# Kernel tuning notes

Measured on AMD Instinct MI355X. Metric: run time of the kernel, lower is better.

## Reference

```python
import jax, jax.numpy as jnp
import numpy as np

EMBED_DIM = 1024
NUM_HEADS = 16
LB_HEADS = 8
LA_HEADS = 8
HEAD_DIM = EMBED_DIM // NUM_HEADS


def setup_inputs() -> dict:
    key = jax.random.key(0)
    ks = jax.random.split(key, 8)
    B, T, F, D = 2, 16, 128, EMBED_DIM
    def xavier(k, shape):
        fan_out, fan_in = shape[-2], shape[-1]
        lim = float(np.sqrt(6.0 / (fan_in + fan_out)))
        return jax.random.uniform(k, shape, jnp.float32, -lim, lim)
    return {
        "x": jax.random.normal(ks[0], (B, T, F, D), jnp.float32),
        # stacked per-head Linear weights, torch layout (out=head_dim, in=D)
        "Wq_lb": xavier(ks[1], (LB_HEADS, HEAD_DIM, D)),
        "Wk_lb": xavier(ks[2], (LB_HEADS, HEAD_DIM, D)),
        "Wv_lb": xavier(ks[3], (LB_HEADS, HEAD_DIM, D)),
        "Wq_la": xavier(ks[4], (LA_HEADS, HEAD_DIM, D)),
        "Wk_la": xavier(ks[5], (LA_HEADS, HEAD_DIM, D)),
        "Wv_la": xavier(ks[6], (LA_HEADS, HEAD_DIM, D)),
        "Wo": xavier(ks[7], (D, D)),
    }


def _masked_attention(xf, Wq, Wk, Wv, lookahead):
    # xf: (B, N, D); W*: (H, E, D). Equivalent to per-head Linear then stack.
    q = jnp.einsum('bnd,hed->bhne', xf, Wq)
    k = jnp.einsum('bnd,hed->bhne', xf, Wk)
    v = jnp.einsum('bnd,hed->bhne', xf, Wv)
    scale = 1.0 / jnp.sqrt(jnp.asarray(q.shape[-1], q.dtype))
    s = jnp.einsum('bhqe,bhke->bhqk', q, k) * scale
    n = s.shape[-1]
    i = jnp.arange(n)
    # frame/patch divmod mask reduces to token-level (anti-)causal
    mask = (i[:, None] <= i[None, :]) if lookahead else (i[:, None] >= i[None, :])
    s = jnp.where(mask, s, jnp.finfo(s.dtype).min)
    p = jax.nn.softmax(s, axis=-1)
    return jnp.einsum('bhqk,bhke->bhqe', p, v)  # (B, H, N, E)


def reference(x, Wq_lb, Wk_lb, Wv_lb, Wq_la, Wk_la, Wv_la, Wo):
    B, T, F, D = x.shape
    xf = x.reshape(B, T * F, D)
    o_lb = _masked_attention(xf, Wq_lb, Wk_lb, Wv_lb, lookahead=False)
    o_la = _masked_attention(xf, Wq_la, Wk_la, Wv_la, lookahead=True)
    o = jnp.concatenate([o_lb, o_la], axis=1)          # (B, H, N, E)
    o = o.reshape(B, T * F, D)                          # NOTE: raw reshape, no head transpose (matches torch source)
    out = jnp.einsum('bnd,od->bno', o, Wo)
    return out.reshape(B, T, F, D)
```

## Files before the change

### kernel.cpp

```cpp
#include <hip/hip_runtime.h>
#include <hip/hip_bf16.h>

constexpr int B_    = 2;
constexpr int NTOK  = 2048;
constexpr int D_    = 1024;
constexpr int H_    = 16;
constexpr int E_    = 64;

using bf16_t = __bf16;
using bf16x8 = __attribute__((ext_vector_type(8))) __bf16;
using f32x4  = __attribute__((ext_vector_type(4))) float;

#define NEG_BIG  (-30000.0f)
#define QSCALE   (0.125f * 1.44269504088896f)

__device__ __forceinline__ void load16_to_lds(const void* g, void* l) {
  __builtin_amdgcn_global_load_lds((const __attribute__((address_space(1))) void*)g,
                                   (__attribute__((address_space(3))) void*)l, 16, 0, 0);
}

__device__ __forceinline__ void stage64_async(const bf16_t* __restrict__ g, int gs,
                                              bf16_t* l, int tid) {
#pragma unroll
  for (int j = 0; j < 2; ++j) {
    int chunk = j * 256 + tid;
    int row = chunk >> 3, cc = chunk & 7;
    int gcc = cc ^ (row & 7);
    load16_to_lds(g + (long)row * gs + gcc * 8, l + chunk * 8);
  }
}

__device__ __forceinline__ void stage128x64_async(const bf16_t* __restrict__ g, int gs,
                                                  bf16_t* l, int tid) {
#pragma unroll
  for (int j = 0; j < 4; ++j) {
    int chunk = j * 256 + tid;
    int row = chunk >> 3, cc = chunk & 7;
    int gcc = cc ^ (row & 7);
    load16_to_lds(g + (long)row * gs + gcc * 8, l + chunk * 8);
  }
}

__device__ __forceinline__ bf16x8 frag_ld(const bf16_t* l, int row, int ks, int half) {
  int cc = (ks * 4 + half) ^ (row & 7);
  return *(const bf16x8*)&l[row * 64 + cc * 8];
}

__device__ __forceinline__ bf16x8 cvt8(f32x4 f0, f32x4 f1) {
  bf16x8 v;
  v[0] = (bf16_t)f0[0]; v[1] = (bf16_t)f0[1]; v[2] = (bf16_t)f0[2]; v[3] = (bf16_t)f0[3];
  v[4] = (bf16_t)f1[0]; v[5] = (bf16_t)f1[1]; v[6] = (bf16_t)f1[2]; v[7] = (bf16_t)f1[3];
  return v;
}

__global__ __launch_bounds__(256) void prep_kernel(
    const float* __restrict__ x,
    const float* __restrict__ q0, const float* __restrict__ q1,
    const float* __restrict__ k0, const float* __restrict__ k1,
    const float* __restrict__ v0, const float* __restrict__ v1,
    const float* __restrict__ wo,
    bf16_t* __restrict__ xb, bf16_t* __restrict__ Wb, bf16_t* __restrict__ Wob)
{
  const int bid = blockIdx.x;
  if (bid < 2048) {
    long i = ((long)bid * 256 + threadIdx.x) * 8;
    *(bf16x8*)&xb[i] = cvt8(*(const f32x4*)&x[i], *(const f32x4*)&x[i + 4]);
  } else if (bid < 3584) {
    int rb = bid - 2048;
    int sec = rb >> 5;
    int qkv = sec >> 4, hh = sec & 15;
    const float* s = (qkv == 0) ? (hh < 8 ? q0 : q1)
                   : (qkv == 1) ? (hh < 8 ? k0 : k1)
                                : (hh < 8 ? v0 : v1);
    s += (long)(hh & 7) * (E_ * D_);
    long off = ((long)(rb & 31) * 256 + threadIdx.x) * 8;
    *(bf16x8*)&Wb[(long)sec * (E_ * D_) + off] =
        cvt8(*(const f32x4*)&s[off], *(const f32x4*)&s[off + 4]);
  } else {
    long i = ((long)(bid - 3584) * 256 + threadIdx.x) * 8;
    *(bf16x8*)&Wob[i] = cvt8(*(const f32x4*)&wo[i], *(const f32x4*)&wo[i + 4]);
  }
}

__global__ __launch_bounds__(256) void qkv128_kernel(
    const bf16_t* __restrict__ xb, const bf16_t* __restrict__ Wb,
    bf16_t* __restrict__ Qb, bf16_t* __restrict__ Kb, bf16_t* __restrict__ Vt)
{
  __shared__ __align__(16) bf16_t smem[2 * 128 * 64];
  bf16_t* As = smem;
  bf16_t* Bs = smem + 128 * 64;

  const int tid = threadIdx.x;
  const int wv = tid >> 6, lane = tid & 63, lane16 = lane & 15, half = lane >> 4;
  const int wm = wv >> 1, wn = wv & 1;
  const int mt = blockIdx.x, nt = blockIdx.y;

  const bf16_t* Ag = xb + (long)mt * 128 * D_;
  const bf16_t* Bg = Wb + (long)nt * 128 * D_;

  f32x4 acc[4][4] = {};

  for (int k0 = 0; k0 < D_; k0 += 64) {
    __syncthreads();
    stage128x64_async(Ag + k0, D_, As, tid);
    stage128x64_async(Bg + k0, D_, Bs, tid);
    __syncthreads();
#pragma unroll
    for (int ks = 0; ks < 2; ++ks) {
      bf16x8 a[4], b[4];
#pragma unroll
      for (int i = 0; i < 4; ++i) a[i] = frag_ld(As, wm * 64 + i * 16 + lane16, ks, half);
#pragma unroll
      for (int i = 0; i < 4; ++i) b[i] = frag_ld(Bs, wn * 64 + i * 16 + lane16, ks, half);
#pragma unroll
      for (int mi = 0; mi < 4; ++mi)
#pragma unroll
        for (int ni = 0; ni < 4; ++ni)
          acc[mi][ni] = __builtin_amdgcn_mfma_f32_16x16x32_bf16(a[mi], b[ni], acc[mi][ni], 0, 0, 0);
    }
  }

  const int sec = nt >> 3;
  const int tok0 = mt * 128;
  const int b  = tok0 >> 11;
  const int n0 = tok0 & 2047;

  if (sec < 2) {
    const float qs = (sec == 0) ? QSCALE : 1.0f;
    bf16_t* dst = (sec == 0) ? Qb : Kb;
#pragma unroll
    for (int mi = 0; mi < 4; ++mi)
#pragma unroll
      for (int ni = 0; ni < 4; ++ni)
#pragma unroll
        for (int r = 0; r < 4; ++r) {
          int row  = wm * 64 + mi * 16 + half * 4 + r;
          int colg = nt * 128 + wn * 64 + ni * 16 + lane16;
          int cs = colg & 1023, h = cs >> 6, e = cs & 63;
          dst[((long)(b * H_ + h) * NTOK + n0 + row) * E_ + e] = (bf16_t)(acc[mi][ni][r] * qs);
        }
  } else {
#pragma unroll
    for (int c = 0; c < 2; ++c) {
      __syncthreads();
      if (wn == c) {
#pragma unroll
        for (int mi = 0; mi < 4; ++mi)
#pragma unroll
          for (int ni = 0; ni < 4; ++ni)
#pragma unroll
            for (int r = 0; r < 4; ++r) {
              int tok = wm * 64 + mi * 16 + half * 4 + r;
              int e   = ni * 16 + lane16;
              smem[e * 136 + tok] = (bf16_t)acc[mi][ni][r];
            }
      }
      __syncthreads();
      int hh = (nt & 7) * 2 + c;
      bf16_t* vdst = Vt + ((long)(b * H_ + hh) * E_) * NTOK;
#pragma unroll
      for (int q = 0; q < 4; ++q) {
        int chunk = q * 256 + tid;
        int e = chunk >> 4, toff = (chunk & 15) * 8;
        *(bf16x8*)&vdst[(long)e * NTOK + n0 + toff] = *(const bf16x8*)&smem[e * 136 + toff];
      }
    }
  }
}

__global__ __launch_bounds__(256) void attn_kernel(
    const bf16_t* __restrict__ Qb, const bf16_t* __restrict__ Kb,
    const bf16_t* __restrict__ Vt, bf16_t* __restrict__ Ob)
{
  __shared__ __align__(16) bf16_t Kl[2][64 * 64];
  __shared__ __align__(16) bf16_t Vl[2][64 * 64];
  __shared__ __align__(16) bf16_t Pl[2][64 * 72];

  const int tid = threadIdx.x;
  const int wv = tid >> 6, lane = tid & 63, lane16 = lane & 15, half = lane >> 4;
  const int qp = blockIdx.x, h = blockIdx.y, b = blockIdx.z;
  const bool causal = (h < 8);
  const int qb[2] = { qp, 31 - qp };
  const long bh = (long)(b * H_ + h);

  bf16x8 qf[2][2];
#pragma unroll
  for (int t = 0; t < 2; ++t) {
    const bf16_t* qg = Qb + (bh * NTOK + (long)qb[t] * 64 + 16 * wv + lane16) * E_;
    qf[t][0] = *(const bf16x8*)(qg + half * 8);
    qf[t][1] = *(const bf16x8*)(qg + 32 + half * 8);
  }

  f32x4 oacc[2][4] = {};
  float l_acc[2][4] = {};

  const int lo = causal ? 0 : qp;
  const int hi = causal ? 31 - qp : 31;

  stage64_async(Kb + (bh * NTOK + (long)lo * 64) * E_, E_, Kl[0], tid);
  stage64_async(Vt + bh * E_ * NTOK + (long)lo * 64, NTOK, Vl[0], tid);

  for (int kb = lo; kb <= hi; ++kb) {
    const int cur = (kb - lo) & 1;
    __syncthreads();
    if (kb < hi) {
      stage64_async(Kb + (bh * NTOK + (long)(kb + 1) * 64) * E_, E_, Kl[cur ^ 1], tid);
      stage64_async(Vt + bh * E_ * NTOK + (long)(kb + 1) * 64, NTOK, Vl[cur ^ 1], tid);
    }

#pragma unroll
    for (int t = 0; t < 2; ++t) {
      const bool act = causal ? (kb <= qb[t]) : (kb >= qb[t]);
      if (!act) continue;

      f32x4 s[4] = {};
#pragma unroll
      for (int ks = 0; ks < 2; ++ks)
#pragma unroll
        for (int n = 0; n < 4; ++n) {
          bf16x8 bk = frag_ld(Kl[cur], 16 * n + lane16, ks, half);
          s[n] = __builtin_amdgcn_mfma_f32_16x16x32_bf16(qf[t][ks], bk, s[n], 0, 0, 0);
        }

      if (kb == qb[t]) {
#pragma unroll
        for (int n = 0; n < 4; ++n) {
          int key = 16 * n + lane16;
#pragma unroll
          for (int r = 0; r < 4; ++r) {
            int q = 16 * wv + half * 4 + r;
            bool ok = causal ? (q >= key) : (q <= key);
            s[n][r] = ok ? s[n][r] : NEG_BIG;
          }
        }
      }

#pragma unroll
      for (int n = 0; n < 4; ++n)
#pragma unroll
        for (int r = 0; r < 4; ++r) {
          float p = exp2f(s[n][r]);
          s[n][r] = p;
          l_acc[t][r] += p;
        }

#pragma unroll
      for (int n = 0; n < 4; ++n)
#pragma unroll
        for (int r = 0; r < 4; ++r)
          Pl[t][(16 * wv + half * 4 + r) * 72 + 16 * n + lane16] = (bf16_t)s[n][r];
      asm volatile("" ::: "memory");

#pragma unroll
      for (int ks = 0; ks < 2; ++ks) {
        bf16x8 ap = *(const bf16x8*)&Pl[t][(16 * wv + lane16) * 72 + ks * 32 + half * 8];
#pragma unroll
        for (int n = 0; n < 4; ++n) {
          bf16x8 bv = frag_ld(Vl[cur], 16 * n + lane16, ks, half);
          oacc[t][n] = __builtin_amdgcn_mfma_f32_16x16x32_bf16(ap, bv, oacc[t][n], 0, 0, 0);
        }
      }
    }
  }

#pragma unroll
  for (int d = 1; d < 16; d <<= 1)
#pragma unroll
    for (int t = 0; t < 2; ++t)
#pragma unroll
      for (int r = 0; r < 4; ++r) l_acc[t][r] += __shfl_xor(l_acc[t][r], d, 64);

#pragma unroll
  for (int t = 0; t < 2; ++t) {
    bf16_t* og = Ob + (bh * NTOK + (long)qb[t] * 64) * E_;
#pragma unroll
    for (int r = 0; r < 4; ++r) {
      float rcp = 1.0f / l_acc[t][r];
      int row = 16 * wv + half * 4 + r;
#pragma unroll
      for (int n = 0; n < 4; ++n)
        og[(long)row * E_ + 16 * n + lane16] = (bf16_t)(oacc[t][n][r] * rcp);
    }
  }
}

__global__ __launch_bounds__(256) void oproj128_kernel(
    const bf16_t* __restrict__ Ob, const bf16_t* __restrict__ Wob,
    float* __restrict__ res)
{
  __shared__ __align__(16) bf16_t smem[2 * 128 * 64];
  bf16_t* As = smem;
  bf16_t* Bs = smem + 128 * 64;

  const int tid = threadIdx.x;
  const int wv = tid >> 6, lane = tid & 63, lane16 = lane & 15, half = lane >> 4;
  const int wm = wv >> 1, wn = wv & 1;
  const int mt = blockIdx.x, nt = blockIdx.y;

  const bf16_t* Ag = Ob  + (long)mt * 128 * D_;
  const bf16_t* Bg = Wob + (long)nt * 128 * D_;

  f32x4 acc[4][4] = {};

  for (int k0 = 0; k0 < D_; k0 += 64) {
    __syncthreads();
    stage128x64_async(Ag + k0, D_, As, tid);
    stage128x64_async(Bg + k0, D_, Bs, tid);
    __syncthreads();
#pragma unroll
    for (int ks = 0; ks < 2; ++ks) {
      bf16x8 a[4], b[4];
#pragma unroll
      for (int i = 0; i < 4; ++i) a[i] = frag_ld(As, wm * 64 + i * 16 + lane16, ks, half);
#pragma unroll
      for (int i = 0; i < 4; ++i) b[i] = frag_ld(Bs, wn * 64 + i * 16 + lane16, ks, half);
#pragma unroll
      for (int mi = 0; mi < 4; ++mi)
#pragma unroll
        for (int ni = 0; ni < 4; ++ni)
          acc[mi][ni] = __builtin_amdgcn_mfma_f32_16x16x32_bf16(a[mi], b[ni], acc[mi][ni], 0, 0, 0);
    }
  }

#pragma unroll
  for (int mi = 0; mi < 4; ++mi)
#pragma unroll
    for (int ni = 0; ni < 4; ++ni)
#pragma unroll
      for (int r = 0; r < 4; ++r) {
        int row = mt * 128 + wm * 64 + mi * 16 + half * 4 + r;
        int col = nt * 128 + wn * 64 + ni * 16 + lane16;
        res[(long)row * D_ + col] = acc[mi][ni][r];
      }
}

__global__ __launch_bounds__(256) void copy_kernel(const float* __restrict__ src,
                                                   float* __restrict__ dst) {
  long i = ((long)blockIdx.x * 256 + threadIdx.x) * 8;
  *(f32x4*)&dst[i]     = *(const f32x4*)&src[i];
  *(f32x4*)&dst[i + 4] = *(const f32x4*)&src[i + 4];
}

extern "C" void kernel_launch(void* const* d_in, const int* in_sizes, int n_in,
                              void* d_out, int out_size, void* d_ws, size_t ws_size,
                              hipStream_t stream) {
  const float* x     = (const float*)d_in[0];
  const float* wq_lb = (const float*)d_in[1];
  const float* wk_lb = (const float*)d_in[2];
  const float* wv_lb = (const float*)d_in[3];
  const float* wq_la = (const float*)d_in[4];
  const float* wk_la = (const float*)d_in[5];
  const float* wv_la = (const float*)d_in[6];
  const float* wo    = (const float*)d_in[7];
  float* out = (float*)d_out;

  const size_t per_buf = (size_t)B_ * H_ * NTOK * E_;

  bf16_t* Qb = (bf16_t*)d_ws;
  bf16_t* Kb = Qb + per_buf;
  bf16_t* Vt = Kb + per_buf;
  float*  res = (float*)d_ws;

  bf16_t* xb  = (bf16_t*)d_out;
  bf16_t* Wb  = xb + per_buf;
  bf16_t* Wob = Wb + (size_t)3 * 1024 * 1024;
  bf16_t* Ob  = (bf16_t*)d_out;

  prep_kernel<<<4096, 256, 0, stream>>>(x, wq_lb, wq_la, wk_lb, wk_la,
                                        wv_lb, wv_la, wo, xb, Wb, Wob);
  qkv128_kernel<<<dim3(32, 24), 256, 0, stream>>>(xb, Wb, Qb, Kb, Vt);
  attn_kernel<<<dim3(16, 16, 2), 256, 0, stream>>>(Qb, Kb, Vt, Ob);
  oproj128_kernel<<<dim3(32, 8), 256, 0, stream>>>(Ob, Wob, res);
  copy_kernel<<<2048, 256, 0, stream>>>(res, out);
}
```

Before: 212.8 us.

## Swap MFMA operands to get transposed accumulators and vectorize epilogue stores

Swaps the A/B operands of the MFMA calls in the Q/K projection, attention and output projection, so each lane's four accumulator values lie along the contiguous feature dimension. Stores then become 4-wide vector writes (bf16x4 or f32x4) instead of scalar scattered writes. In attention, the row sum becomes one scalar per lane, cutting the cross-lane shuffle reduction to two steps. K and V fragments are hoisted out of the per-tile loop so both query tiles share them. The V transpose staging in LDS changes row padding from 136 to 144 to fit the new write pattern.

```diff
diff --git a/kernel.cpp b/kernel.cpp
--- a/kernel.cpp
+++ b/kernel.cpp
@@ -9,6 +9,7 @@
 
 using bf16_t = __bf16;
 using bf16x8 = __attribute__((ext_vector_type(8))) __bf16;
+using bf16x4 = __attribute__((ext_vector_type(4))) __bf16;
 using f32x4  = __attribute__((ext_vector_type(4))) float;
 
 #define NEG_BIG  (-30000.0f)
@@ -50,6 +51,13 @@
   bf16x8 v;
   v[0] = (bf16_t)f0[0]; v[1] = (bf16_t)f0[1]; v[2] = (bf16_t)f0[2]; v[3] = (bf16_t)f0[3];
   v[4] = (bf16_t)f1[0]; v[5] = (bf16_t)f1[1]; v[6] = (bf16_t)f1[2]; v[7] = (bf16_t)f1[3];
+  return v;
+}
+
+__device__ __forceinline__ bf16x4 cvt4(f32x4 f, float sc) {
+  bf16x4 v;
+  v[0] = (bf16_t)(f[0] * sc); v[1] = (bf16_t)(f[1] * sc);
+  v[2] = (bf16_t)(f[2] * sc); v[3] = (bf16_t)(f[3] * sc);
   return v;
 }
 
@@ -94,33 +102,55 @@
   const int wv = tid >> 6, lane = tid & 63, lane16 = lane & 15, half = lane >> 4;
   const int wm = wv >> 1, wn = wv & 1;
   const int mt = blockIdx.x, nt = blockIdx.y;
+  const int sec = nt >> 3;
 
   const bf16_t* Ag = xb + (long)mt * 128 * D_;
   const bf16_t* Bg = Wb + (long)nt * 128 * D_;
 
   f32x4 acc[4][4] = {};
 
-  for (int k0 = 0; k0 < D_; k0 += 64) {
-    __syncthreads();
-    stage128x64_async(Ag + k0, D_, As, tid);
-    stage128x64_async(Bg + k0, D_, Bs, tid);
-    __syncthreads();
-#pragma unroll
-    for (int ks = 0; ks < 2; ++ks) {
-      bf16x8 a[4], b[4];
-#pragma unroll
-      for (int i = 0; i < 4; ++i) a[i] = frag_ld(As, wm * 64 + i * 16 + lane16, ks, half);
-#pragma unroll
-      for (int i = 0; i < 4; ++i) b[i] = frag_ld(Bs, wn * 64 + i * 16 + lane16, ks, half);
-#pragma unroll
-      for (int mi = 0; mi < 4; ++mi)
-#pragma unroll
-        for (int ni = 0; ni < 4; ++ni)
-          acc[mi][ni] = __builtin_amdgcn_mfma_f32_16x16x32_bf16(a[mi], b[ni], acc[mi][ni], 0, 0, 0);
-    }
-  }
-
-  const int sec = nt >> 3;
+  if (sec < 2) {
+    for (int k0 = 0; k0 < D_; k0 += 64) {
+      __syncthreads();
+      stage128x64_async(Ag + k0, D_, As, tid);
+      stage128x64_async(Bg + k0, D_, Bs, tid);
+      __syncthreads();
+#pragma unroll
+      for (int ks = 0; ks < 2; ++ks) {
+        bf16x8 a[4], b[4];
+#pragma unroll
+        for (int i = 0; i < 4; ++i) a[i] = frag_ld(As, wm * 64 + i * 16 + lane16, ks, half);
+#pragma unroll
+        for (int i = 0; i < 4; ++i) b[i] = frag_ld(Bs, wn * 64 + i * 16 + lane16, ks, half);
+#pragma unroll
+        for (int mi = 0; mi < 4; ++mi)
+#pragma unroll
+          for (int ni = 0; ni < 4; ++ni)
+            acc[mi][ni] = __builtin_amdgcn_mfma_f32_16x16x32_bf16(b[ni], a[mi], acc[mi][ni], 0, 0, 0);
+      }
+    }
+  } else {
+    for (int k0 = 0; k0 < D_; k0 += 64) {
+      __syncthreads();
+      stage128x64_async(Ag + k0, D_, As, tid);
+      stage128x64_async(Bg + k0, D_, Bs, tid);
+      __syncthreads();
+#pragma unroll
+      for (int ks = 0; ks < 2; ++ks) {
+        bf16x8 a[4], b[4];
+#pragma unroll
+        for (int i = 0; i < 4; ++i) a[i] = frag_ld(As, wm * 64 + i * 16 + lane16, ks, half);
+#pragma unroll
+        for (int i = 0; i < 4; ++i) b[i] = frag_ld(Bs, wn * 64 + i * 16 + lane16, ks, half);
+#pragma unroll
+        for (int mi = 0; mi < 4; ++mi)
+#pragma unroll
+          for (int ni = 0; ni < 4; ++ni)
+            acc[mi][ni] = __builtin_amdgcn_mfma_f32_16x16x32_bf16(a[mi], b[ni], acc[mi][ni], 0, 0, 0);
+      }
+    }
+  }
+
   const int tok0 = mt * 128;
   const int b  = tok0 >> 11;
   const int n0 = tok0 & 2047;
@@ -131,14 +161,13 @@
 #pragma unroll
     for (int mi = 0; mi < 4; ++mi)
 #pragma unroll
-      for (int ni = 0; ni < 4; ++ni)
-#pragma unroll
-        for (int r = 0; r < 4; ++r) {
-          int row  = wm * 64 + mi * 16 + half * 4 + r;
-          int colg = nt * 128 + wn * 64 + ni * 16 + lane16;
-          int cs = colg & 1023, h = cs >> 6, e = cs & 63;
-          dst[((long)(b * H_ + h) * NTOK + n0 + row) * E_ + e] = (bf16_t)(acc[mi][ni][r] * qs);
-        }
+      for (int ni = 0; ni < 4; ++ni) {
+        int token = wm * 64 + 16 * mi + lane16;
+        int colg  = nt * 128 + wn * 64 + 16 * ni + half * 4;
+        int cs = colg & 1023, hh = cs >> 6, e0 = cs & 63;
+        *(bf16x4*)&dst[((long)(b * H_ + hh) * NTOK + n0 + token) * E_ + e0] =
+            cvt4(acc[mi][ni], qs);
+      }
   } else {
 #pragma unroll
     for (int c = 0; c < 2; ++c) {
@@ -147,13 +176,11 @@
 #pragma unroll
         for (int mi = 0; mi < 4; ++mi)
 #pragma unroll
-          for (int ni = 0; ni < 4; ++ni)
-#pragma unroll
-            for (int r = 0; r < 4; ++r) {
-              int tok = wm * 64 + mi * 16 + half * 4 + r;
-              int e   = ni * 16 + lane16;
-              smem[e * 136 + tok] = (bf16_t)acc[mi][ni][r];
-            }
+          for (int ni = 0; ni < 4; ++ni) {
+            int t0v = wm * 64 + 16 * mi + half * 4;
+            int e   = 16 * ni + lane16;
+            *(bf16x4*)&smem[e * 144 + t0v] = cvt4(acc[mi][ni], 1.0f);
+          }
       }
       __syncthreads();
       int hh = (nt & 7) * 2 + c;
@@ -162,7 +189,7 @@
       for (int q = 0; q < 4; ++q) {
         int chunk = q * 256 + tid;
         int e = chunk >> 4, toff = (chunk & 15) * 8;
-        *(bf16x8*)&vdst[(long)e * NTOK + n0 + toff] = *(const bf16x8*)&smem[e * 136 + toff];
+        *(bf16x8*)&vdst[(long)e * NTOK + n0 + toff] = *(const bf16x8*)&smem[e * 144 + toff];
       }
     }
   }
@@ -182,17 +209,18 @@
   const bool causal = (h < 8);
   const int qb[2] = { qp, 31 - qp };
   const long bh = (long)(b * H_ + h);
+  const int qrow = 16 * wv + lane16;
 
   bf16x8 qf[2][2];
 #pragma unroll
   for (int t = 0; t < 2; ++t) {
-    const bf16_t* qg = Qb + (bh * NTOK + (long)qb[t] * 64 + 16 * wv + lane16) * E_;
+    const bf16_t* qg = Qb + (bh * NTOK + (long)qb[t] * 64 + qrow) * E_;
     qf[t][0] = *(const bf16x8*)(qg + half * 8);
     qf[t][1] = *(const bf16x8*)(qg + 32 + half * 8);
   }
 
   f32x4 oacc[2][4] = {};
-  float l_acc[2][4] = {};
+  float l_acc[2] = { 0.f, 0.f };
 
   const int lo = causal ? 0 : qp;
   const int hi = causal ? 31 - qp : 31;
@@ -207,80 +235,88 @@
       stage64_async(Kb + (bh * NTOK + (long)(kb + 1) * 64) * E_, E_, Kl[cur ^ 1], tid);
       stage64_async(Vt + bh * E_ * NTOK + (long)(kb + 1) * 64, NTOK, Vl[cur ^ 1], tid);
     }
+    const bool act[2] = { causal ? (kb <= qb[0]) : (kb >= qb[0]),
+                          causal ? (kb <= qb[1]) : (kb >= qb[1]) };
+
+    bf16x8 kfr[2][4];
+#pragma unroll
+    for (int ks = 0; ks < 2; ++ks)
+#pragma unroll
+      for (int n = 0; n < 4; ++n)
+        kfr[ks][n] = frag_ld(Kl[cur], 16 * n + lane16, ks, half);
 
 #pragma unroll
     for (int t = 0; t < 2; ++t) {
-      const bool act = causal ? (kb <= qb[t]) : (kb >= qb[t]);
-      if (!act) continue;
-
+      if (!act[t]) continue;
       f32x4 s[4] = {};
 #pragma unroll
       for (int ks = 0; ks < 2; ++ks)
 #pragma unroll
-        for (int n = 0; n < 4; ++n) {
-          bf16x8 bk = frag_ld(Kl[cur], 16 * n + lane16, ks, half);
-          s[n] = __builtin_amdgcn_mfma_f32_16x16x32_bf16(qf[t][ks], bk, s[n], 0, 0, 0);
-        }
+        for (int n = 0; n < 4; ++n)
+          s[n] = __builtin_amdgcn_mfma_f32_16x16x32_bf16(kfr[ks][n], qf[t][ks], s[n], 0, 0, 0);
 
       if (kb == qb[t]) {
 #pragma unroll
-        for (int n = 0; n < 4; ++n) {
-          int key = 16 * n + lane16;
+        for (int n = 0; n < 4; ++n)
 #pragma unroll
           for (int r = 0; r < 4; ++r) {
-            int q = 16 * wv + half * 4 + r;
-            bool ok = causal ? (q >= key) : (q <= key);
+            int key = 16 * n + half * 4 + r;
+            bool ok = causal ? (qrow >= key) : (qrow <= key);
             s[n][r] = ok ? s[n][r] : NEG_BIG;
           }
-        }
-      }
-
+      }
+
+      float lsum = 0.f;
 #pragma unroll
       for (int n = 0; n < 4; ++n)
 #pragma unroll
         for (int r = 0; r < 4; ++r) {
           float p = exp2f(s[n][r]);
           s[n][r] = p;
-          l_acc[t][r] += p;
+          lsum += p;
         }
-
-#pragma unroll
-      for (int n = 0; n < 4; ++n)
-#pragma unroll
-        for (int r = 0; r < 4; ++r)
-          Pl[t][(16 * wv + half * 4 + r) * 72 + 16 * n + lane16] = (bf16_t)s[n][r];
-      asm volatile("" ::: "memory");
-
-#pragma unroll
-      for (int ks = 0; ks < 2; ++ks) {
-        bf16x8 ap = *(const bf16x8*)&Pl[t][(16 * wv + lane16) * 72 + ks * 32 + half * 8];
-#pragma unroll
-        for (int n = 0; n < 4; ++n) {
-          bf16x8 bv = frag_ld(Vl[cur], 16 * n + lane16, ks, half);
-          oacc[t][n] = __builtin_amdgcn_mfma_f32_16x16x32_bf16(ap, bv, oacc[t][n], 0, 0, 0);
-        }
-      }
-    }
-  }
-
-#pragma unroll
-  for (int d = 1; d < 16; d <<= 1)
-#pragma unroll
-    for (int t = 0; t < 2; ++t)
-#pragma unroll
-      for (int r = 0; r < 4; ++r) l_acc[t][r] += __shfl_xor(l_acc[t][r], d, 64);
+      l_acc[t] += lsum;
+
+#pragma unroll
+      for (int n = 0; n < 4; ++n)
+        *(bf16x4*)&Pl[t][qrow * 72 + 16 * n + half * 4] = cvt4(s[n], 1.0f);
+    }
+    asm volatile("" ::: "memory");
+
+    bf16x8 vfr[2][4];
+#pragma unroll
+    for (int ks = 0; ks < 2; ++ks)
+#pragma unroll
+      for (int n = 0; n < 4; ++n)
+        vfr[ks][n] = frag_ld(Vl[cur], 16 * n + lane16, ks, half);
+
+#pragma unroll
+    for (int t = 0; t < 2; ++t) {
+      if (!act[t]) continue;
+      bf16x8 ap0 = *(const bf16x8*)&Pl[t][qrow * 72 + half * 8];
+      bf16x8 ap1 = *(const bf16x8*)&Pl[t][qrow * 72 + 32 + half * 8];
+#pragma unroll
+      for (int n = 0; n < 4; ++n)
+        oacc[t][n] = __builtin_amdgcn_mfma_f32_16x16x32_bf16(vfr[0][n], ap0, oacc[t][n], 0, 0, 0);
+#pragma unroll
+      for (int n = 0; n < 4; ++n)
+        oacc[t][n] = __builtin_amdgcn_mfma_f32_16x16x32_bf16(vfr[1][n], ap1, oacc[t][n], 0, 0, 0);
+    }
+  }
 
 #pragma unroll
   for (int t = 0; t < 2; ++t) {
-    bf16_t* og = Ob + (bh * NTOK + (long)qb[t] * 64) * E_;
-#pragma unroll
-    for (int r = 0; r < 4; ++r) {
-      float rcp = 1.0f / l_acc[t][r];
-      int row = 16 * wv + half * 4 + r;
-#pragma unroll
-      for (int n = 0; n < 4; ++n)
-        og[(long)row * E_ + 16 * n + lane16] = (bf16_t)(oacc[t][n][r] * rcp);
-    }
+    l_acc[t] += __shfl_xor(l_acc[t], 16, 64);
+    l_acc[t] += __shfl_xor(l_acc[t], 32, 64);
+  }
+
+#pragma unroll
+  for (int t = 0; t < 2; ++t) {
+    float rcp = 1.0f / l_acc[t];
+    bf16_t* og = Ob + (bh * NTOK + (long)qb[t] * 64 + qrow) * E_;
+#pragma unroll
+    for (int n = 0; n < 4; ++n)
+      *(bf16x4*)&og[16 * n + half * 4] = cvt4(oacc[t][n], rcp);
   }
 }
 
@@ -318,20 +354,18 @@
       for (int mi = 0; mi < 4; ++mi)
 #pragma unroll
         for (int ni = 0; ni < 4; ++ni)
-          acc[mi][ni] = __builtin_amdgcn_mfma_f32_16x16x32_bf16(a[mi], b[ni], acc[mi][ni], 0, 0, 0);
+          acc[mi][ni] = __builtin_amdgcn_mfma_f32_16x16x32_bf16(b[ni], a[mi], acc[mi][ni], 0, 0, 0);
     }
   }
 
 #pragma unroll
   for (int mi = 0; mi < 4; ++mi)
 #pragma unroll
-    for (int ni = 0; ni < 4; ++ni)
-#pragma unroll
-      for (int r = 0; r < 4; ++r) {
-        int row = mt * 128 + wm * 64 + mi * 16 + half * 4 + r;
-        int col = nt * 128 + wn * 64 + ni * 16 + lane16;
-        res[(long)row * D_ + col] = acc[mi][ni][r];
-      }
+    for (int ni = 0; ni < 4; ++ni) {
+      int row  = mt * 128 + wm * 64 + 16 * mi + lane16;
+      int col0 = nt * 128 + wn * 64 + 16 * ni + half * 4;
+      *(f32x4*)&res[(long)row * D_ + col0] = acc[mi][ni];
+    }
 }
 
 __global__ __launch_bounds__(256) void copy_kernel(const float* __restrict__ src,
```

After: 212.5 us. Within noise of the previous version (-0.2%).
